# Optimization experiments

Hardware: AMD Instinct MI355X
Metric: run time of the kernel (lower is better)

## Reference

```python
import jax, jax.numpy as jnp
import numpy as np

B, H, W = 16, 1024, 1024
EPS = 1e-7
FG_PROB = 0.1  # foreground pixel probability for synthetic gt


def setup_inputs() -> dict:
    key = jax.random.key(0)
    k1, k2 = jax.random.split(key)
    probs = jax.random.normal(k1, (B, 2, H, W), dtype=jnp.float32)
    gt = (jax.random.uniform(k2, (B, H, W)) < FG_PROB).astype(jnp.float32)
    gt_f_num = gt.sum(axis=(1, 2))  # per-sample foreground pixel count (float)
    return {"probs": probs, "gt": gt, "gt_f_num": gt_f_num, "img_h": H, "img_w": W}


def reference(probs, gt, gt_f_num, img_h, img_w):
    # foreground probability, clamped
    pc = jax.nn.softmax(probs, axis=1)[:, 1, :, :]
    pc = jnp.clip(pc, EPS, 1.0 - EPS)
    b = pc.shape[0]
    f_loss = -(gt * jnp.log(pc)).reshape(b, -1)          # [B, N]
    b_loss = -((1.0 - gt) * jnp.log(1.0 - pc)).reshape(b, -1)  # [B, N]
    n = b_loss.shape[1]

    # sort background loss descending per sample; top gt_f_num[i] entries are
    # "difficult" negatives, the rest are "simple" (equivalent to the torch
    # gather-into-zero-buffers since only sums/counts are taken afterwards)
    sorted_b = -jnp.sort(-b_loss, axis=1)                # descending, [B, N]
    k = gt_f_num.astype(jnp.int32)                       # int(gt_f_num[i])
    mask = jnp.arange(n, dtype=jnp.int32)[None, :] < k[:, None]  # [B, N]

    difficult_sum = jnp.sum(jnp.where(mask, sorted_b, 0.0), axis=1)
    simple_sum = jnp.sum(jnp.where(mask, 0.0, sorted_b), axis=1)
    difficult_num = jnp.sum(mask & (sorted_b != 0.0), axis=1).astype(jnp.float32)

    difficult_b_loss = difficult_sum / (difficult_num + 1e-16)
    simple_b_loss = simple_sum / (float(img_h * img_w) + 1e-16)
    f_loss_mean = f_loss.sum(axis=1) / (gt_f_num + 1e-16)

    return difficult_b_loss.mean() + f_loss_mean.mean() + simple_b_loss.mean()
```

## Files before the change

kernel.cpp:

```cpp
#include <hip/hip_runtime.h>
#include <math.h>

#define NB 16
#define NPIX 1048576
#define BINS 4096
#define CHUNKS 64
#define TPB_A 512
#define PIX_PER_BLOCK (NPIX / CHUNKS)
#define PPT 8
#define ITERS_A (PIX_PER_BLOCK / (TPB_A * PPT))
#define TPB_B 256
#define BINS_PER_CHUNK (BINS / TPB_B)
#define BLOSS_MAX 16.2f
#define BINW (BLOSS_MAX / (float)BINS)
#define B_CAP 15.9424f
#define F_CAP 16.1181f

__device__ __forceinline__ void fadd_glb(float* p, float v) {
    __hip_atomic_fetch_add(p, v, __ATOMIC_RELAXED, __HIP_MEMORY_SCOPE_AGENT);
}

__global__ __launch_bounds__(TPB_A) void pass_a(
    const float* __restrict__ probs, const float* __restrict__ gt,
    unsigned* __restrict__ g_cnt, float* __restrict__ f_sum,
    float* __restrict__ b_sum)
{
    __shared__ unsigned s_cnt[BINS];
    __shared__ float s_redf[TPB_A / 64];
    __shared__ float s_redb[TPB_A / 64];

    const int tid = threadIdx.x;
    for (int j = tid; j < BINS; j += TPB_A) s_cnt[j] = 0u;
    __syncthreads();

    const int blk = blockIdx.x;
    const int b = blk / CHUNKS;
    const int chunk = blk % CHUNKS;
    const float* p0 = probs + (size_t)b * 2 * NPIX;
    const float* p1 = p0 + NPIX;
    const float* gp = gt + (size_t)b * NPIX;
    const int base = chunk * PIX_PER_BLOCK;
    const float scale = (float)BINS / BLOSS_MAX;

    float f_acc = 0.f, b_acc = 0.f;

    float4 cA0, cB0, cA1, cB1, cG0, cG1;
    {
        const int i = base + (tid << 2);
        const int i2 = i + TPB_A * 4;
        cA0 = *(const float4*)(p0 + i);  cB0 = *(const float4*)(p0 + i2);
        cA1 = *(const float4*)(p1 + i);  cB1 = *(const float4*)(p1 + i2);
        cG0 = *(const float4*)(gp + i);  cG1 = *(const float4*)(gp + i2);
    }
    for (int it = 0; it < ITERS_A; ++it) {
        float4 nA0, nB0, nA1, nB1, nG0, nG1;
        {
            const int nit = (it + 1 < ITERS_A) ? it + 1 : it;
            const int i = base + nit * (TPB_A * PPT) + (tid << 2);
            const int i2 = i + TPB_A * 4;
            nA0 = *(const float4*)(p0 + i);  nB0 = *(const float4*)(p0 + i2);
            nA1 = *(const float4*)(p1 + i);  nB1 = *(const float4*)(p1 + i2);
            nG0 = *(const float4*)(gp + i);  nG1 = *(const float4*)(gp + i2);
        }
        const float dv[PPT] = {cA1.x - cA0.x, cA1.y - cA0.y, cA1.z - cA0.z, cA1.w - cA0.w,
                               cB1.x - cB0.x, cB1.y - cB0.y, cB1.z - cB0.z, cB1.w - cB0.w};
        const float gv[PPT] = {cG0.x, cG0.y, cG0.z, cG0.w, cG1.x, cG1.y, cG1.z, cG1.w};
        #pragma unroll
        for (int q = 0; q < PPT; ++q) {
            const float d = dv[q];
            const float sp = fmaxf(d, 0.f) + __logf(1.f + __expf(-fabsf(d)));
            if (gv[q] > 0.5f) {
                f_acc += fminf(sp - d, F_CAP);
            } else {
                const float bl = fminf(sp, B_CAP);
                b_acc += bl;
                int bin = (int)(bl * scale);
                bin = bin < (BINS - 1) ? bin : (BINS - 1);
                atomicAdd(&s_cnt[bin], 1u);
            }
        }
        cA0 = nA0; cB0 = nB0; cA1 = nA1; cB1 = nB1; cG0 = nG0; cG1 = nG1;
    }
    __syncthreads();

    for (int j = tid; j < BINS; j += TPB_A) {
        const unsigned c = s_cnt[j];
        if (c) atomicAdd(&g_cnt[(size_t)b * BINS + j], c);
    }

    #pragma unroll
    for (int o = 32; o > 0; o >>= 1) {
        f_acc += __shfl_down(f_acc, o, 64);
        b_acc += __shfl_down(b_acc, o, 64);
    }
    if ((tid & 63) == 0) { s_redf[tid >> 6] = f_acc; s_redb[tid >> 6] = b_acc; }
    __syncthreads();
    if (tid == 0) {
        float f = 0.f, bs = 0.f;
        #pragma unroll
        for (int w = 0; w < TPB_A / 64; ++w) { f += s_redf[w]; bs += s_redb[w]; }
        fadd_glb(&f_sum[b], f);
        fadd_glb(&b_sum[b], bs);
    }
}

__global__ __launch_bounds__(TPB_B) void pass_b(
    const unsigned* __restrict__ g_cnt, const float* __restrict__ f_sum,
    const float* __restrict__ b_sum, const float* __restrict__ gt_f_num,
    float* __restrict__ terms)
{
    __shared__ unsigned s_cnt[BINS];
    __shared__ unsigned s_suf[TPB_B];
    __shared__ double s_wsuf[TPB_B];
    __shared__ double s_dsum;

    const int b = blockIdx.x;
    const int t = threadIdx.x;

    for (int j = 0; j < BINS_PER_CHUNK; ++j) {
        const int bin = j * TPB_B + t;
        s_cnt[bin] = g_cnt[(size_t)b * BINS + bin];
    }
    __syncthreads();

    unsigned c = 0; double w = 0.0;
    const int cb = t * BINS_PER_CHUNK;
    for (int j = 0; j < BINS_PER_CHUNK; ++j) {
        const unsigned cc = s_cnt[cb + j];
        c += cc;
        w += (double)cc * (double)(((float)(cb + j) + 0.5f) * BINW);
    }
    s_suf[t] = c; s_wsuf[t] = w;
    __syncthreads();

    for (int off = 1; off < TPB_B; off <<= 1) {
        const unsigned ac = (t + off < TPB_B) ? s_suf[t + off] : 0u;
        const double aw = (t + off < TPB_B) ? s_wsuf[t + off] : 0.0;
        __syncthreads();
        s_suf[t] += ac; s_wsuf[t] += aw;
        __syncthreads();
    }

    const long long kk = (long long)gt_f_num[b];
    const unsigned long long n_pos = (unsigned long long)s_suf[0];
    const unsigned long long suf_me = s_suf[t];
    const unsigned long long suf_nx = (t + 1 < TPB_B) ? s_suf[t + 1] : 0ull;

    if (kk > 0 && (unsigned long long)kk < n_pos &&
        suf_nx < (unsigned long long)kk && (unsigned long long)kk <= suf_me) {
        unsigned long long cum = suf_nx;
        double W = (t + 1 < TPB_B) ? s_wsuf[t + 1] : 0.0;
        int bstar = cb;
        for (int j = BINS_PER_CHUNK - 1; j >= 0; --j) {
            const int bin = cb + j;
            const unsigned cc = s_cnt[bin];
            if (cum + cc >= (unsigned long long)kk) { bstar = bin; break; }
            cum += cc;
            W += (double)cc * (double)(((float)bin + 0.5f) * BINW);
        }
        const double partial = (double)(kk - (long long)cum);
        s_dsum = W + partial * (double)(((float)bstar + 0.5f) * BINW);
    }
    __syncthreads();

    if (t == 0) {
        const double S_total = (double)b_sum[b];
        const double fs = (double)f_sum[b];
        const double gfn = (double)gt_f_num[b];
        double dsum, dnum;
        if (kk <= 0) { dsum = 0.0; dnum = 0.0; }
        else if ((unsigned long long)kk >= n_pos) { dsum = S_total; dnum = (double)n_pos; }
        else { dsum = s_dsum; dnum = (double)kk; }
        const double term = dsum / (dnum + 1e-16)
                          + fs / (gfn + 1e-16)
                          + (S_total - dsum) / ((double)NPIX + 1e-16);
        terms[b] = (float)term;
    }
}

__global__ void pass_c(const float* __restrict__ terms, float* __restrict__ out)
{
    if (threadIdx.x == 0 && blockIdx.x == 0) {
        float s = 0.f;
        #pragma unroll
        for (int i = 0; i < NB; ++i) s += terms[i];
        out[0] = s / (float)NB;
    }
}

extern "C" void kernel_launch(void* const* d_in, const int* in_sizes, int n_in,
                              void* d_out, int out_size, void* d_ws, size_t ws_size,
                              hipStream_t stream) {
    const float* probs = (const float*)d_in[0];
    const float* gt    = (const float*)d_in[1];
    const float* gfn   = (const float*)d_in[2];
    char* ws = (char*)d_ws;

    const size_t hist_bytes = (size_t)NB * BINS * 4;
    unsigned* g_cnt = (unsigned*)ws;
    float*    f_sum = (float*)(ws + hist_bytes);
    float*    b_sum = f_sum + NB;
    float*    terms = b_sum + NB;

    hipMemsetAsync(ws, 0, hist_bytes + 2 * NB * sizeof(float), stream);

    hipLaunchKernelGGL(pass_a, dim3(NB * CHUNKS), dim3(TPB_A), 0, stream,
                       probs, gt, g_cnt, f_sum, b_sum);
    hipLaunchKernelGGL(pass_b, dim3(NB), dim3(TPB_B), 0, stream,
                       g_cnt, f_sum, b_sum, gfn, terms);
    hipLaunchKernelGGL(pass_c, dim3(1), dim3(64), 0, stream,
                       terms, (float*)d_out);
}
```

Baseline: 243.9 us.

## Write per-block packed 16-bit histograms and partials instead of global atomics

After: 251.6 us. 3.2% more time.

```diff
diff --git a/kernel.cpp b/kernel.cpp
--- a/kernel.cpp
+++ b/kernel.cpp
@@ -4,6 +4,7 @@
 #define NB 16
 #define NPIX 1048576
 #define BINS 4096
+#define HBINS (BINS / 2)
 #define CHUNKS 64
 #define TPB_A 512
 #define PIX_PER_BLOCK (NPIX / CHUNKS)
@@ -11,26 +12,23 @@
 #define ITERS_A (PIX_PER_BLOCK / (TPB_A * PPT))
 #define TPB_B 256
 #define BINS_PER_CHUNK (BINS / TPB_B)
+#define WORDS_PER_THREAD (HBINS / TPB_B)
 #define BLOSS_MAX 16.2f
 #define BINW (BLOSS_MAX / (float)BINS)
 #define B_CAP 15.9424f
 #define F_CAP 16.1181f
 
-__device__ __forceinline__ void fadd_glb(float* p, float v) {
-    __hip_atomic_fetch_add(p, v, __ATOMIC_RELAXED, __HIP_MEMORY_SCOPE_AGENT);
-}
-
 __global__ __launch_bounds__(TPB_A) void pass_a(
     const float* __restrict__ probs, const float* __restrict__ gt,
-    unsigned* __restrict__ g_cnt, float* __restrict__ f_sum,
-    float* __restrict__ b_sum)
+    unsigned* __restrict__ g_hist, float* __restrict__ f_part,
+    float* __restrict__ b_part)
 {
-    __shared__ unsigned s_cnt[BINS];
+    __shared__ unsigned s_cnt[HBINS];
     __shared__ float s_redf[TPB_A / 64];
     __shared__ float s_redb[TPB_A / 64];
 
     const int tid = threadIdx.x;
-    for (int j = tid; j < BINS; j += TPB_A) s_cnt[j] = 0u;
+    for (int j = tid; j < HBINS; j += TPB_A) s_cnt[j] = 0u;
     __syncthreads();
 
     const int blk = blockIdx.x;
@@ -76,17 +74,15 @@
                 b_acc += bl;
                 int bin = (int)(bl * scale);
                 bin = bin < (BINS - 1) ? bin : (BINS - 1);
-                atomicAdd(&s_cnt[bin], 1u);
+                atomicAdd(&s_cnt[bin >> 1], 1u << ((bin & 1) << 4));
             }
         }
         cA0 = nA0; cB0 = nB0; cA1 = nA1; cB1 = nB1; cG0 = nG0; cG1 = nG1;
     }
     __syncthreads();
 
-    for (int j = tid; j < BINS; j += TPB_A) {
-        const unsigned c = s_cnt[j];
-        if (c) atomicAdd(&g_cnt[(size_t)b * BINS + j], c);
-    }
+    unsigned* dst = g_hist + ((size_t)b * CHUNKS + chunk) * HBINS;
+    for (int j = tid; j < HBINS; j += TPB_A) dst[j] = s_cnt[j];
 
     #pragma unroll
     for (int o = 32; o > 0; o >>= 1) {
@@ -99,38 +95,61 @@
         float f = 0.f, bs = 0.f;
         #pragma unroll
         for (int w = 0; w < TPB_A / 64; ++w) { f += s_redf[w]; bs += s_redb[w]; }
-        fadd_glb(&f_sum[b], f);
-        fadd_glb(&b_sum[b], bs);
+        f_part[b * CHUNKS + chunk] = f;
+        b_part[b * CHUNKS + chunk] = bs;
     }
 }
 
 __global__ __launch_bounds__(TPB_B) void pass_b(
-    const unsigned* __restrict__ g_cnt, const float* __restrict__ f_sum,
-    const float* __restrict__ b_sum, const float* __restrict__ gt_f_num,
+    const unsigned* __restrict__ g_hist, const float* __restrict__ f_part,
+    const float* __restrict__ b_part, const float* __restrict__ gt_f_num,
     float* __restrict__ terms)
 {
-    __shared__ unsigned s_cnt[BINS];
     __shared__ unsigned s_suf[TPB_B];
     __shared__ double s_wsuf[TPB_B];
     __shared__ double s_dsum;
+    __shared__ double s_fb[2];
 
     const int b = blockIdx.x;
     const int t = threadIdx.x;
 
+    unsigned cnt[BINS_PER_CHUNK];
+    #pragma unroll
+    for (int j = 0; j < BINS_PER_CHUNK; ++j) cnt[j] = 0u;
+    const unsigned* hb = g_hist + (size_t)b * CHUNKS * HBINS + t * WORDS_PER_THREAD;
+    #pragma unroll 4
+    for (int c = 0; c < CHUNKS; ++c) {
+        const uint4 w0 = *(const uint4*)(hb + (size_t)c * HBINS);
+        const uint4 w1 = *(const uint4*)(hb + (size_t)c * HBINS + 4);
+        cnt[0]  += w0.x & 0xFFFFu;  cnt[1]  += w0.x >> 16;
+        cnt[2]  += w0.y & 0xFFFFu;  cnt[3]  += w0.y >> 16;
+        cnt[4]  += w0.z & 0xFFFFu;  cnt[5]  += w0.z >> 16;
+        cnt[6]  += w0.w & 0xFFFFu;  cnt[7]  += w0.w >> 16;
+        cnt[8]  += w1.x & 0xFFFFu;  cnt[9]  += w1.x >> 16;
+        cnt[10] += w1.y & 0xFFFFu;  cnt[11] += w1.y >> 16;
+        cnt[12] += w1.z & 0xFFFFu;  cnt[13] += w1.z >> 16;
+        cnt[14] += w1.w & 0xFFFFu;  cnt[15] += w1.w >> 16;
+    }
+
+    const int cb = t * BINS_PER_CHUNK;
+    unsigned c = 0; double w = 0.0;
+    #pragma unroll
     for (int j = 0; j < BINS_PER_CHUNK; ++j) {
-        const int bin = j * TPB_B + t;
-        s_cnt[bin] = g_cnt[(size_t)b * BINS + bin];
-    }
-    __syncthreads();
-
-    unsigned c = 0; double w = 0.0;
-    const int cb = t * BINS_PER_CHUNK;
-    for (int j = 0; j < BINS_PER_CHUNK; ++j) {
-        const unsigned cc = s_cnt[cb + j];
-        c += cc;
-        w += (double)cc * (double)(((float)(cb + j) + 0.5f) * BINW);
+        c += cnt[j];
+        w += (double)cnt[j] * (double)(((float)(cb + j) + 0.5f) * BINW);
     }
     s_suf[t] = c; s_wsuf[t] = w;
+
+    if (t < 64) {
+        double ff = (double)f_part[b * CHUNKS + t];
+        double bb = (double)b_part[b * CHUNKS + t];
+        #pragma unroll
+        for (int o = 32; o > 0; o >>= 1) {
+            ff += __shfl_down(ff, o, 64);
+            bb += __shfl_down(bb, o, 64);
+        }
+        if (t == 0) { s_fb[0] = ff; s_fb[1] = bb; }
+    }
     __syncthreads();
 
     for (int off = 1; off < TPB_B; off <<= 1) {
@@ -152,11 +171,10 @@
         double W = (t + 1 < TPB_B) ? s_wsuf[t + 1] : 0.0;
         int bstar = cb;
         for (int j = BINS_PER_CHUNK - 1; j >= 0; --j) {
-            const int bin = cb + j;
-            const unsigned cc = s_cnt[bin];
-            if (cum + cc >= (unsigned long long)kk) { bstar = bin; break; }
+            const unsigned cc = cnt[j];
+            if (cum + cc >= (unsigned long long)kk) { bstar = cb + j; break; }
             cum += cc;
-            W += (double)cc * (double)(((float)bin + 0.5f) * BINW);
+            W += (double)cc * (double)(((float)(cb + j) + 0.5f) * BINW);
         }
         const double partial = (double)(kk - (long long)cum);
         s_dsum = W + partial * (double)(((float)bstar + 0.5f) * BINW);
@@ -164,8 +182,8 @@
     __syncthreads();
 
     if (t == 0) {
-        const double S_total = (double)b_sum[b];
-        const double fs = (double)f_sum[b];
+        const double S_total = s_fb[1];
+        const double fs = s_fb[0];
         const double gfn = (double)gt_f_num[b];
         double dsum, dnum;
         if (kk <= 0) { dsum = 0.0; dnum = 0.0; }
@@ -196,18 +214,16 @@
     const float* gfn   = (const float*)d_in[2];
     char* ws = (char*)d_ws;
 
-    const size_t hist_bytes = (size_t)NB * BINS * 4;
-    unsigned* g_cnt = (unsigned*)ws;
-    float*    f_sum = (float*)(ws + hist_bytes);
-    float*    b_sum = f_sum + NB;
-    float*    terms = b_sum + NB;
-
-    hipMemsetAsync(ws, 0, hist_bytes + 2 * NB * sizeof(float), stream);
+    const size_t hist_bytes = (size_t)NB * CHUNKS * HBINS * sizeof(unsigned);
+    unsigned* g_hist = (unsigned*)ws;
+    float*    f_part = (float*)(ws + hist_bytes);
+    float*    b_part = f_part + NB * CHUNKS;
+    float*    terms  = b_part + NB * CHUNKS;
 
     hipLaunchKernelGGL(pass_a, dim3(NB * CHUNKS), dim3(TPB_A), 0, stream,
-                       probs, gt, g_cnt, f_sum, b_sum);
+                       probs, gt, g_hist, f_part, b_part);
     hipLaunchKernelGGL(pass_b, dim3(NB), dim3(TPB_B), 0, stream,
-                       g_cnt, f_sum, b_sum, gfn, terms);
+                       g_hist, f_part, b_part, gfn, terms);
     hipLaunchKernelGGL(pass_c, dim3(1), dim3(64), 0, stream,
                        terms, (float*)d_out);
 }
```
